# Performance work log

Measured on AMD Instinct MI355X. Metric: run time of the kernel, lower is better.

Reference implementation:

```python
import jax, jax.numpy as jnp
import numpy as np

N = 100000
E = 1600000
IN_DIM = 64
HID = 64


def _glorot(key, shape):
    fan_in, fan_out = shape[0], shape[1]
    lim = np.sqrt(6.0 / (fan_in + fan_out))
    return jax.random.uniform(key, shape, jnp.float32, -lim, lim)


def setup_inputs() -> dict:
    key = jax.random.key(0)
    ks = jax.random.split(key, 14)
    x = jax.random.normal(ks[0], (N, IN_DIM), jnp.float32)
    edge_index = jax.random.randint(ks[1], (2, E), 0, N, jnp.int64)
    dims = [(IN_DIM, HID), (HID, HID), (HID, HID), (HID, 1)]
    inp = {"x": x, "edge_index": edge_index}
    for i, (di, do) in enumerate(dims, start=1):
        inp[f"Wself{i}"] = _glorot(ks[2 + 3 * (i - 1)], (di, do))
        inp[f"Wneigh{i}"] = _glorot(ks[3 + 3 * (i - 1)], (di, do))
        inp[f"b{i}"] = jnp.zeros((do,), jnp.float32)
    return inp


def _gn_block(h, src, dst, deg_inv, Wself, Wneigh, b, act):
    # gather -> scatter-add -> mean -> dense transform (GraphConv-style)
    msg = h[src]                                           # [E, d]
    agg = jax.ops.segment_sum(msg, dst, num_segments=N)    # [N, d]
    agg = agg * deg_inv                                    # mean aggregation
    out = h @ Wself + agg @ Wneigh + b
    return act(out)


def reference(x, edge_index, Wself1, Wneigh1, b1, Wself2, Wneigh2, b2,
              Wself3, Wneigh3, b3, Wself4, Wneigh4, b4):
    src, dst = edge_index[0], edge_index[1]
    deg = jax.ops.segment_sum(jnp.ones((E,), x.dtype), dst, num_segments=N)
    deg_inv = (1.0 / jnp.maximum(deg, 1.0))[:, None]       # [N, 1]
    relu = jax.nn.relu
    h = _gn_block(x, src, dst, deg_inv, Wself1, Wneigh1, b1, relu)
    h = _gn_block(h, src, dst, deg_inv, Wself2, Wneigh2, b2, relu)
    h = _gn_block(h, src, dst, deg_inv, Wself3, Wneigh3, b3, relu)
    h = _gn_block(h, src, dst, deg_inv, Wself4, Wneigh4, b4, lambda z: z)
    return jax.nn.sigmoid(h)                               # [N, 1]
```

## Files before the change

kernel.cpp:

```cpp
#include <hip/hip_runtime.h>
#include <hip/hip_bf16.h>
#include <math.h>


using bfrag = __attribute__((ext_vector_type(8))) short;
using ffrag = __attribute__((ext_vector_type(4))) float;

#define BKT_SHIFT 9
#define BKT_NODES (1 << BKT_SHIFT)
#define AGG_F_STRIDE 65

__device__ __forceinline__ int load_idx32(const int* __restrict__ ei32, int is64,
                                          long long pos) {
    return is64 ? ei32[2 * pos] : ei32[pos];
}

__device__ __forceinline__ unsigned short f2b_rne(float f) {
    union { float f; unsigned u; } c;
    c.f = f;
    unsigned r = c.u + 0x7FFFu + ((c.u >> 16) & 1u);
    return (unsigned short)(r >> 16);
}

__device__ __forceinline__ float b2f(unsigned short u) {
    union { unsigned u; float f; } c;
    c.u = ((unsigned)u) << 16;
    return c.f;
}

__global__ void bprep_init_kernel(
    const float* __restrict__ Ws1, const float* __restrict__ Wn1,
    const float* __restrict__ Ws2, const float* __restrict__ Wn2,
    const float* __restrict__ Ws3, const float* __restrict__ Wn3,
    unsigned short* __restrict__ bthi, unsigned short* __restrict__ btlo,
    const int* __restrict__ ei, int* __restrict__ bktc, int* __restrict__ flag) {
    if (blockIdx.x == 0) {
        bktc[threadIdx.x] = 0;
        if (threadIdx.x == 0) {
            int allz = 1;
            for (int i = 0; i < 32; ++i)
                if (ei[2 * i + 1] != 0) allz = 0;
            *flag = allz;
        }
    }
    int i = blockIdx.x * 256 + threadIdx.x;
    if (i >= 3 * 8192) return;
    int layer = i >> 13;
    int j = i & 8191;
    int n = j >> 7, k = j & 127;
    const float* Ws = layer == 0 ? Ws1 : (layer == 1 ? Ws2 : Ws3);
    const float* Wn = layer == 0 ? Wn1 : (layer == 1 ? Wn2 : Wn3);
    float v = (k < 64) ? Ws[k * 64 + n] : Wn[(k - 64) * 64 + n];
    unsigned short hi = f2b_rne(v);
    bthi[i] = hi;
    btlo[i] = f2b_rne(v - b2f(hi));
}

__global__ void split_x_kernel(const float4* __restrict__ in, ushort4* __restrict__ hi,
                               int n4) {
    int i = blockIdx.x * blockDim.x + threadIdx.x;
    if (i >= n4) return;
    float4 v = in[i];
    ushort4 h;
    h.x = f2b_rne(v.x); h.y = f2b_rne(v.y); h.z = f2b_rne(v.z); h.w = f2b_rne(v.w);
    hi[i] = h;
}

__global__ __launch_bounds__(256) void binA_kernel(
    const int* __restrict__ ei32, const int* __restrict__ flagp,
    int* __restrict__ bktCnt, unsigned* __restrict__ bins, int E, int nbkt,
    int cap, int chunksz) {
    __shared__ int cnt[256];
    __shared__ int base[256];
    int is64 = *flagp;
    int elo = blockIdx.x * chunksz;
    int ehi = min(E, elo + chunksz);
    if (elo >= E) return;
    for (int i = threadIdx.x; i < nbkt; i += 256) cnt[i] = 0;
    __syncthreads();
    for (int e = elo + (int)threadIdx.x; e < ehi; e += 256) {
        int dst = load_idx32(ei32, is64, (long long)E + e);
        atomicAdd(&cnt[dst >> BKT_SHIFT], 1);
    }
    __syncthreads();
    for (int i = threadIdx.x; i < nbkt; i += 256) {
        base[i] = atomicAdd(&bktCnt[i], cnt[i]);
        cnt[i] = 0;
    }
    __syncthreads();
    for (int e = elo + (int)threadIdx.x; e < ehi; e += 256) {
        int dst = load_idx32(ei32, is64, (long long)E + e);
        int src = load_idx32(ei32, is64, e);
        int b = dst >> BKT_SHIFT;
        int r = atomicAdd(&cnt[b], 1);
        bins[(size_t)b * cap + base[b] + r] =
            ((unsigned)(dst & (BKT_NODES - 1)) << 23) | (unsigned)src;
    }
}

__global__ __launch_bounds__(256) void bucketCSR_kernel(
    const int* __restrict__ bktCnt, const unsigned* __restrict__ bins,
    int2* __restrict__ offp, int* __restrict__ col,
    float* __restrict__ dinv, int N, int cap) {
    __shared__ int deg[BKT_NODES];
    __shared__ int loc[BKT_NODES];
    __shared__ int ssum[256];
    int b = blockIdx.x;
    int lo = b << BKT_SHIFT;
    int n = min(BKT_NODES, N - lo);
    for (int i = threadIdx.x; i < BKT_NODES; i += 256) deg[i] = 0;
    __syncthreads();
    int cnt = bktCnt[b];
    const unsigned* bb = bins + (size_t)b * cap;
    for (int i = threadIdx.x; i < cnt; i += 256)
        atomicAdd(&deg[bb[i] >> 23], 1);
    __syncthreads();
    int t = threadIdx.x;
    int d0 = deg[2 * t], d1 = deg[2 * t + 1];
    int s = d0 + d1;
    ssum[t] = s;
    __syncthreads();
    for (int o = 1; o < 256; o <<= 1) {
        int v = (t >= o) ? ssum[t - o] : 0;
        __syncthreads();
        ssum[t] += v;
        __syncthreads();
    }
    int excl = ssum[t] - s;
    loc[2 * t] = excl;
    loc[2 * t + 1] = excl + d0;
    __syncthreads();
    int base = b * cap;
    for (int i = threadIdx.x; i < n; i += 256) {
        int d = deg[i];
        offp[lo + i] = make_int2(base + loc[i], base + loc[i] + d);
        dinv[lo + i] = 1.0f / fmaxf((float)d, 1.0f);
    }
    __syncthreads();
    for (int i = threadIdx.x; i < cnt; i += 256) {
        unsigned p = bb[i];
        int pos = atomicAdd(&loc[p >> 23], 1);
        col[base + pos] = (int)(p & 0x7FFFFFu);
    }
}

__device__ __forceinline__ void acc4(float4& a, ushort4 u) {
    a.x += b2f(u.x); a.y += b2f(u.y); a.z += b2f(u.z); a.w += b2f(u.w);
}

__device__ __forceinline__ void fma4(float4& a, float m, ushort4 u) {
    a.x = fmaf(m, b2f(u.x), a.x);
    a.y = fmaf(m, b2f(u.y), a.y);
    a.z = fmaf(m, b2f(u.z), a.z);
    a.w = fmaf(m, b2f(u.w), a.w);
}

__device__ __forceinline__ void gather_half(
    const unsigned short* __restrict__ Hhi, const int* __restrict__ col,
    float* __restrict__ dstF, int e, int end, int t16) {
    float4 a0 = make_float4(0.f, 0.f, 0.f, 0.f);
    float4 a1 = a0, a2 = a0, a3 = a0;
    const unsigned short* __restrict__ Hq = Hhi + t16 * 4;
    for (; e + 8 <= end; e += 8) {
        int s0 = col[e + 0], s1 = col[e + 1], s2 = col[e + 2], s3 = col[e + 3];
        int s4 = col[e + 4], s5 = col[e + 5], s6 = col[e + 6], s7 = col[e + 7];
        ushort4 u0 = *(const ushort4*)&Hq[(size_t)s0 * 64];
        ushort4 u1 = *(const ushort4*)&Hq[(size_t)s1 * 64];
        ushort4 u2 = *(const ushort4*)&Hq[(size_t)s2 * 64];
        ushort4 u3 = *(const ushort4*)&Hq[(size_t)s3 * 64];
        ushort4 u4 = *(const ushort4*)&Hq[(size_t)s4 * 64];
        ushort4 u5 = *(const ushort4*)&Hq[(size_t)s5 * 64];
        ushort4 u6 = *(const ushort4*)&Hq[(size_t)s6 * 64];
        ushort4 u7 = *(const ushort4*)&Hq[(size_t)s7 * 64];
        acc4(a0, u0); acc4(a1, u1); acc4(a2, u2); acc4(a3, u3);
        acc4(a0, u4); acc4(a1, u5); acc4(a2, u6); acc4(a3, u7);
    }
    int rem = end - e;
    if (rem > 0) {
        int last = end - 1;
#pragma unroll
        for (int j = 0; j < 7; ++j) {
            int idx = e + j;
            int cl = idx < last ? idx : last;
            int s = col[cl];
            ushort4 u = *(const ushort4*)&Hq[(size_t)s * 64];
            float m = (j < rem) ? 1.0f : 0.0f;
            if ((j & 3) == 0) fma4(a0, m, u);
            else if ((j & 3) == 1) fma4(a1, m, u);
            else if ((j & 3) == 2) fma4(a2, m, u);
            else fma4(a3, m, u);
        }
    }
    float4 s;
    s.x = (a0.x + a1.x) + (a2.x + a3.x);
    s.y = (a0.y + a1.y) + (a2.y + a3.y);
    s.z = (a0.z + a1.z) + (a2.z + a3.z);
    s.w = (a0.w + a1.w) + (a2.w + a3.w);
    *(float4*)&dstF[t16 * 4] = s;
}

__device__ __forceinline__ bfrag cvt8(const float* __restrict__ p0,
                                      const float* __restrict__ p1, float di) {
    bfrag r;
#pragma unroll
    for (int i = 0; i < 8; ++i)
        r[i] = (short)f2b_rne((p0[i] + p1[i]) * di);
    return r;
}

__global__ __launch_bounds__(512, 8) void layer_fused_kernel(
    const unsigned short* __restrict__ Hhi, const int2* __restrict__ offp,
    const int* __restrict__ col, const float* __restrict__ dinv,
    const unsigned short* __restrict__ Bthi, const unsigned short* __restrict__ Btlo,
    const float* __restrict__ b, unsigned short* __restrict__ Dhi, int N) {
    __shared__ float aggF[32 * AGG_F_STRIDE];
    int wave = threadIdx.x >> 6;
    int lane = threadIdx.x & 63;
    int g = lane >> 4;
    int t16 = lane & 15;
    int n0 = blockIdx.x * 16;
    int grp = wave * 4 + g;
    int li = grp >> 1, half = grp & 1;
    int n = n0 + li;
    int e0 = 0, e1 = 0;
    if (n < N) {
        int2 oo = offp[n];
        int d = oo.y - oo.x;
        int c0 = (d + 1) >> 1;
        e0 = half ? oo.x + c0 : oo.x;
        e1 = half ? oo.y : oo.x + c0;
    }
    gather_half(Hhi, col, &aggF[grp * AGG_F_STRIDE], e0, e1, t16);
    __syncthreads();
    if (wave < 4) {
        int m = t16, quad = g;
        int nr = n0 + m;
        if (nr > N - 1) nr = N - 1;
        float di = dinv[nr];
        const float* r0 = &aggF[(m * 2 + 0) * AGG_F_STRIDE];
        const float* r1 = &aggF[(m * 2 + 1) * AGG_F_STRIDE];
        const unsigned short* hrow = Hhi + (size_t)nr * 64 + quad * 8;
        bfrag ah[4];
        ah[0] = *(const bfrag*)(hrow);
        ah[1] = *(const bfrag*)(hrow + 32);
        ah[2] = cvt8(r0 + quad * 8, r1 + quad * 8, di);
        ah[3] = cvt8(r0 + 32 + quad * 8, r1 + 32 + quad * 8, di);
        int oc = wave * 16 + m;
        float bl = b[oc];
        ffrag acc = {bl, bl, bl, bl};
#pragma unroll
        for (int c = 0; c < 4; ++c) {
            bfrag bh = *(const bfrag*)(Bthi + (size_t)oc * 128 + c * 32 + quad * 8);
            bfrag bw = *(const bfrag*)(Btlo + (size_t)oc * 128 + c * 32 + quad * 8);
            acc = __builtin_amdgcn_mfma_f32_16x16x32_bf16(ah[c], bh, acc, 0, 0, 0);
            acc = __builtin_amdgcn_mfma_f32_16x16x32_bf16(ah[c], bw, acc, 0, 0, 0);
        }
#pragma unroll
        for (int r = 0; r < 4; ++r) {
            int node = n0 + quad * 4 + r;
            if (node < N)
                Dhi[(size_t)node * 64 + oc] = f2b_rne(fmaxf(acc[r], 0.f));
        }
    }
}

__global__ __launch_bounds__(512, 8) void layer_fused_last_kernel(
    const unsigned short* __restrict__ Hhi, const int2* __restrict__ offp,
    const int* __restrict__ col, const float* __restrict__ dinv,
    const unsigned short* __restrict__ Bthi, const unsigned short* __restrict__ Btlo,
    const float* __restrict__ b, const float* __restrict__ Ws4,
    const float* __restrict__ Wn4, float* __restrict__ sbuf,
    float* __restrict__ gbuf, int N) {
    __shared__ float aggF[32 * AGG_F_STRIDE];
    __shared__ float sPart[4][16];
    __shared__ float gPart[4][16];
    int wave = threadIdx.x >> 6;
    int lane = threadIdx.x & 63;
    int g = lane >> 4;
    int t16 = lane & 15;
    int n0 = blockIdx.x * 16;
    int grp = wave * 4 + g;
    int li = grp >> 1, half = grp & 1;
    int n = n0 + li;
    int e0 = 0, e1 = 0;
    if (n < N) {
        int2 oo = offp[n];
        int d = oo.y - oo.x;
        int c0 = (d + 1) >> 1;
        e0 = half ? oo.x + c0 : oo.x;
        e1 = half ? oo.y : oo.x + c0;
    }
    gather_half(Hhi, col, &aggF[grp * AGG_F_STRIDE], e0, e1, t16);
    __syncthreads();
    if (wave < 4) {
        int m = t16, quad = g;
        int nr = n0 + m;
        if (nr > N - 1) nr = N - 1;
        float di = dinv[nr];
        const float* r0 = &aggF[(m * 2 + 0) * AGG_F_STRIDE];
        const float* r1 = &aggF[(m * 2 + 1) * AGG_F_STRIDE];
        const unsigned short* hrow = Hhi + (size_t)nr * 64 + quad * 8;
        bfrag ah[4];
        ah[0] = *(const bfrag*)(hrow);
        ah[1] = *(const bfrag*)(hrow + 32);
        ah[2] = cvt8(r0 + quad * 8, r1 + quad * 8, di);
        ah[3] = cvt8(r0 + 32 + quad * 8, r1 + 32 + quad * 8, di);
        int oc = wave * 16 + m;
        float bl = b[oc];
        ffrag acc = {bl, bl, bl, bl};
#pragma unroll
        for (int c = 0; c < 4; ++c) {
            bfrag bh = *(const bfrag*)(Bthi + (size_t)oc * 128 + c * 32 + quad * 8);
            bfrag bw = *(const bfrag*)(Btlo + (size_t)oc * 128 + c * 32 + quad * 8);
            acc = __builtin_amdgcn_mfma_f32_16x16x32_bf16(ah[c], bh, acc, 0, 0, 0);
            acc = __builtin_amdgcn_mfma_f32_16x16x32_bf16(ah[c], bw, acc, 0, 0, 0);
        }
        float w4s = Ws4[oc], w4n = Wn4[oc];
#pragma unroll
        for (int r = 0; r < 4; ++r) {
            float v = fmaxf(acc[r], 0.f);
            float ps = v * w4s;
            float pg = v * w4n;
#pragma unroll
            for (int mask = 1; mask <= 8; mask <<= 1) {
                ps += __shfl_xor(ps, mask, 64);
                pg += __shfl_xor(pg, mask, 64);
            }
            if (m == 0) {
                sPart[wave][quad * 4 + r] = ps;
                gPart[wave][quad * 4 + r] = pg;
            }
        }
    }
    __syncthreads();
    if (threadIdx.x < 16) {
        int node = n0 + threadIdx.x;
        if (node < N) {
            float s = sPart[0][threadIdx.x] + sPart[1][threadIdx.x] +
                      sPart[2][threadIdx.x] + sPart[3][threadIdx.x];
            float gg = gPart[0][threadIdx.x] + gPart[1][threadIdx.x] +
                       gPart[2][threadIdx.x] + gPart[3][threadIdx.x];
            sbuf[node] = s;
            gbuf[node] = gg;
        }
    }
}

__global__ void final_kernel(const float* __restrict__ s, const float* __restrict__ dinv,
                             const float* __restrict__ g, const int2* __restrict__ offp,
                             const int* __restrict__ col,
                             const float* __restrict__ b4, float* __restrict__ out, int N) {
    int n = blockIdx.x * blockDim.x + threadIdx.x;
    if (n >= N) return;
    float a = 0.f;
    int2 oo = offp[n];
    for (int e = oo.x; e < oo.y; ++e) a += g[col[e]];
    float z = s[n] + dinv[n] * a + b4[0];
    out[n] = 1.0f / (1.0f + expf(-z));
}

static inline int cdiv(long long a, long long b) { return (int)((a + b - 1) / b); }

extern "C" void kernel_launch(void* const* d_in, const int* in_sizes, int n_in,
                              void* d_out, int out_size, void* d_ws, size_t ws_size,
                              hipStream_t stream) {
    const float* x   = (const float*)d_in[0];
    const int*   ei  = (const int*)d_in[1];
    const float* Ws1 = (const float*)d_in[2];
    const float* Wn1 = (const float*)d_in[3];
    const float* b1  = (const float*)d_in[4];
    const float* Ws2 = (const float*)d_in[5];
    const float* Wn2 = (const float*)d_in[6];
    const float* b2  = (const float*)d_in[7];
    const float* Ws3 = (const float*)d_in[8];
    const float* Wn3 = (const float*)d_in[9];
    const float* b3  = (const float*)d_in[10];
    const float* Ws4 = (const float*)d_in[11];
    const float* Wn4 = (const float*)d_in[12];
    const float* b4  = (const float*)d_in[13];
    float* out = (float*)d_out;

    const int N = in_sizes[0] / 64;
    const int E = in_sizes[1] / 2;

    const int nbkt = cdiv(N, BKT_NODES);
    int cap = E / nbkt + E / nbkt / 8 + 64;
    cap = (cap + 1) & ~1;

    unsigned* bins = (unsigned*)d_ws;
    int* col = (int*)(bins + (size_t)nbkt * cap);
    int2* offp = (int2*)(col + (size_t)nbkt * cap);
    unsigned short* HhiA = (unsigned short*)(offp + N);
    unsigned short* HhiB = HhiA + (size_t)N * 64;
    unsigned short* Bth  = HhiB + (size_t)N * 64;
    unsigned short* Btl  = Bth + 3 * 8192;
    float* dinv = (float*)(Btl + 3 * 8192);
    float* sbuf = dinv + N;
    float* gbuf = sbuf + N;
    int*   bktc = (int*)(gbuf + N);
    int*   flag = bktc + 256;

    const int BT = 256;
    const int gridN  = cdiv(N, BT);
    const int gridL  = cdiv(N, 16);
    const int binBlocks = 512;
    const int chunksz = cdiv(E, binBlocks);

    bprep_init_kernel<<<96, BT, 0, stream>>>(Ws1, Wn1, Ws2, Wn2, Ws3, Wn3,
                                             Bth, Btl, ei, bktc, flag);
    split_x_kernel<<<cdiv((long long)N * 16, BT), BT, 0, stream>>>(
        (const float4*)x, (ushort4*)HhiA, N * 16);

    binA_kernel<<<binBlocks, BT, 0, stream>>>(ei, flag, bktc, bins, E, nbkt, cap, chunksz);
    bucketCSR_kernel<<<nbkt, BT, 0, stream>>>(bktc, bins, offp, col, dinv, N, cap);

    layer_fused_kernel<<<gridL, 512, 0, stream>>>(HhiA, offp, col, dinv,
                                                  Bth, Btl, b1, HhiB, N);
    layer_fused_kernel<<<gridL, 512, 0, stream>>>(HhiB, offp, col, dinv,
                                                  Bth + 8192, Btl + 8192, b2, HhiA, N);
    layer_fused_last_kernel<<<gridL, 512, 0, stream>>>(HhiA, offp, col, dinv,
                                                       Bth + 16384, Btl + 16384, b3,
                                                       Ws4, Wn4, sbuf, gbuf, N);

    final_kernel<<<gridN, BT, 0, stream>>>(sbuf, dinv, gbuf, offp, col, b4, out, N);
}
```

Baseline: 343.2 us.

## Replace bucketed binning CSR build with global histogram, scan, atomic scatter

Swaps the two-pass bucket-binning CSR construction (shared-memory bucket counts, staged bins array, per-bucket local sort) for a plain global-degree histogram, a two-level prefix scan, and an atomic-cursor scatter into col. This drops the intermediate bins buffer and its extra read/write pass. In exchange it adds more kernel launches and relies on global atomics spread across many destinations, which can contend. The order of neighbours within each row becomes nondeterministic, and the scattered writes no longer stay within a bucket's region, so the layer kernels may see less favourable locality.

```diff
diff --git a/kernel.cpp b/kernel.cpp
--- a/kernel.cpp
+++ b/kernel.cpp
@@ -6,8 +6,6 @@
 using bfrag = __attribute__((ext_vector_type(8))) short;
 using ffrag = __attribute__((ext_vector_type(4))) float;
 
-#define BKT_SHIFT 9
-#define BKT_NODES (1 << BKT_SHIFT)
 #define AGG_F_STRIDE 65
 
 __device__ __forceinline__ int load_idx32(const int* __restrict__ ei32, int is64,
@@ -28,20 +26,20 @@
     return c.f;
 }
 
-__global__ void bprep_init_kernel(
+__global__ __launch_bounds__(256) void bprep_init_kernel(
     const float* __restrict__ Ws1, const float* __restrict__ Wn1,
     const float* __restrict__ Ws2, const float* __restrict__ Wn2,
     const float* __restrict__ Ws3, const float* __restrict__ Wn3,
     unsigned short* __restrict__ bthi, unsigned short* __restrict__ btlo,
-    const int* __restrict__ ei, int* __restrict__ bktc, int* __restrict__ flag) {
-    if (blockIdx.x == 0) {
-        bktc[threadIdx.x] = 0;
-        if (threadIdx.x == 0) {
-            int allz = 1;
-            for (int i = 0; i < 32; ++i)
-                if (ei[2 * i + 1] != 0) allz = 0;
-            *flag = allz;
-        }
+    const int* __restrict__ ei, int* __restrict__ deg, int* __restrict__ flag,
+    int N) {
+    for (int j = blockIdx.x * 256 + threadIdx.x; j < N; j += gridDim.x * 256)
+        deg[j] = 0;
+    if (blockIdx.x == 0 && threadIdx.x == 0) {
+        int allz = 1;
+        for (int i = 0; i < 32; ++i)
+            if (ei[2 * i + 1] != 0) allz = 0;
+        *flag = allz;
     }
     int i = blockIdx.x * 256 + threadIdx.x;
     if (i >= 3 * 8192) return;
@@ -56,8 +54,8 @@
     btlo[i] = f2b_rne(v - b2f(hi));
 }
 
-__global__ void split_x_kernel(const float4* __restrict__ in, ushort4* __restrict__ hi,
-                               int n4) {
+__global__ __launch_bounds__(256) void split_x_kernel(
+    const float4* __restrict__ in, ushort4* __restrict__ hi, int n4) {
     int i = blockIdx.x * blockDim.x + threadIdx.x;
     if (i >= n4) return;
     float4 v = in[i];
@@ -66,81 +64,73 @@
     hi[i] = h;
 }
 
-__global__ __launch_bounds__(256) void binA_kernel(
+__global__ __launch_bounds__(256) void hist_kernel(
     const int* __restrict__ ei32, const int* __restrict__ flagp,
-    int* __restrict__ bktCnt, unsigned* __restrict__ bins, int E, int nbkt,
-    int cap, int chunksz) {
-    __shared__ int cnt[256];
-    __shared__ int base[256];
+    int* __restrict__ deg, int E) {
     int is64 = *flagp;
-    int elo = blockIdx.x * chunksz;
-    int ehi = min(E, elo + chunksz);
-    if (elo >= E) return;
-    for (int i = threadIdx.x; i < nbkt; i += 256) cnt[i] = 0;
+    for (int e = blockIdx.x * 256 + threadIdx.x; e < E; e += gridDim.x * 256) {
+        int dst = load_idx32(ei32, is64, (long long)E + e);
+        atomicAdd(&deg[dst], 1);
+    }
+}
+
+__global__ __launch_bounds__(512) void scan1_kernel(
+    const int* __restrict__ deg, int* __restrict__ locOff,
+    int* __restrict__ btot, int N) {
+    __shared__ int s[512];
+    int b = blockIdx.x, t = threadIdx.x;
+    int n = b * 512 + t;
+    int d = (n < N) ? deg[n] : 0;
+    s[t] = d;
     __syncthreads();
-    for (int e = elo + (int)threadIdx.x; e < ehi; e += 256) {
-        int dst = load_idx32(ei32, is64, (long long)E + e);
-        atomicAdd(&cnt[dst >> BKT_SHIFT], 1);
-    }
-    __syncthreads();
-    for (int i = threadIdx.x; i < nbkt; i += 256) {
-        base[i] = atomicAdd(&bktCnt[i], cnt[i]);
-        cnt[i] = 0;
-    }
-    __syncthreads();
-    for (int e = elo + (int)threadIdx.x; e < ehi; e += 256) {
-        int dst = load_idx32(ei32, is64, (long long)E + e);
-        int src = load_idx32(ei32, is64, e);
-        int b = dst >> BKT_SHIFT;
-        int r = atomicAdd(&cnt[b], 1);
-        bins[(size_t)b * cap + base[b] + r] =
-            ((unsigned)(dst & (BKT_NODES - 1)) << 23) | (unsigned)src;
-    }
-}
-
-__global__ __launch_bounds__(256) void bucketCSR_kernel(
-    const int* __restrict__ bktCnt, const unsigned* __restrict__ bins,
-    int2* __restrict__ offp, int* __restrict__ col,
-    float* __restrict__ dinv, int N, int cap) {
-    __shared__ int deg[BKT_NODES];
-    __shared__ int loc[BKT_NODES];
-    __shared__ int ssum[256];
-    int b = blockIdx.x;
-    int lo = b << BKT_SHIFT;
-    int n = min(BKT_NODES, N - lo);
-    for (int i = threadIdx.x; i < BKT_NODES; i += 256) deg[i] = 0;
-    __syncthreads();
-    int cnt = bktCnt[b];
-    const unsigned* bb = bins + (size_t)b * cap;
-    for (int i = threadIdx.x; i < cnt; i += 256)
-        atomicAdd(&deg[bb[i] >> 23], 1);
-    __syncthreads();
+    for (int o = 1; o < 512; o <<= 1) {
+        int v = (t >= o) ? s[t - o] : 0;
+        __syncthreads();
+        s[t] += v;
+        __syncthreads();
+    }
+    if (n < N) locOff[n] = s[t] - d;
+    if (t == 511) btot[b] = s[t];
+}
+
+__global__ __launch_bounds__(256) void scan2_kernel(
+    const int* __restrict__ btot, int* __restrict__ bbase, int nb) {
+    __shared__ int s[256];
     int t = threadIdx.x;
-    int d0 = deg[2 * t], d1 = deg[2 * t + 1];
-    int s = d0 + d1;
-    ssum[t] = s;
+    int d = (t < nb) ? btot[t] : 0;
+    s[t] = d;
     __syncthreads();
     for (int o = 1; o < 256; o <<= 1) {
-        int v = (t >= o) ? ssum[t - o] : 0;
+        int v = (t >= o) ? s[t - o] : 0;
         __syncthreads();
-        ssum[t] += v;
+        s[t] += v;
         __syncthreads();
     }
-    int excl = ssum[t] - s;
-    loc[2 * t] = excl;
-    loc[2 * t + 1] = excl + d0;
-    __syncthreads();
-    int base = b * cap;
-    for (int i = threadIdx.x; i < n; i += 256) {
-        int d = deg[i];
-        offp[lo + i] = make_int2(base + loc[i], base + loc[i] + d);
-        dinv[lo + i] = 1.0f / fmaxf((float)d, 1.0f);
-    }
-    __syncthreads();
-    for (int i = threadIdx.x; i < cnt; i += 256) {
-        unsigned p = bb[i];
-        int pos = atomicAdd(&loc[p >> 23], 1);
-        col[base + pos] = (int)(p & 0x7FFFFFu);
+    if (t < nb) bbase[t] = s[t] - d;
+}
+
+__global__ __launch_bounds__(256) void finalize_kernel(
+    const int* __restrict__ deg, const int* __restrict__ locOff,
+    const int* __restrict__ bbase, int2* __restrict__ offp,
+    int* __restrict__ cur, float* __restrict__ dinv, int N) {
+    int n = blockIdx.x * 256 + threadIdx.x;
+    if (n >= N) return;
+    int d = deg[n];
+    int start = locOff[n] + bbase[n >> 9];
+    offp[n] = make_int2(start, start + d);
+    cur[n] = start;
+    dinv[n] = 1.0f / fmaxf((float)d, 1.0f);
+}
+
+__global__ __launch_bounds__(256) void scatter_kernel(
+    const int* __restrict__ ei32, const int* __restrict__ flagp,
+    int* __restrict__ cur, int* __restrict__ col, int E) {
+    int is64 = *flagp;
+    for (int e = blockIdx.x * 256 + threadIdx.x; e < E; e += gridDim.x * 256) {
+        int src = load_idx32(ei32, is64, e);
+        int dst = load_idx32(ei32, is64, (long long)E + e);
+        int p = atomicAdd(&cur[dst], 1);
+        col[p] = src;
     }
 }
 
@@ -346,10 +336,11 @@
     }
 }
 
-__global__ void final_kernel(const float* __restrict__ s, const float* __restrict__ dinv,
-                             const float* __restrict__ g, const int2* __restrict__ offp,
-                             const int* __restrict__ col,
-                             const float* __restrict__ b4, float* __restrict__ out, int N) {
+__global__ __launch_bounds__(256) void final_kernel(
+    const float* __restrict__ s, const float* __restrict__ dinv,
+    const float* __restrict__ g, const int2* __restrict__ offp,
+    const int* __restrict__ col,
+    const float* __restrict__ b4, float* __restrict__ out, int N) {
     int n = blockIdx.x * blockDim.x + threadIdx.x;
     if (n >= N) return;
     float a = 0.f;
@@ -382,37 +373,39 @@
 
     const int N = in_sizes[0] / 64;
     const int E = in_sizes[1] / 2;
-
-    const int nbkt = cdiv(N, BKT_NODES);
-    int cap = E / nbkt + E / nbkt / 8 + 64;
-    cap = (cap + 1) & ~1;
-
-    unsigned* bins = (unsigned*)d_ws;
-    int* col = (int*)(bins + (size_t)nbkt * cap);
-    int2* offp = (int2*)(col + (size_t)nbkt * cap);
-    unsigned short* HhiA = (unsigned short*)(offp + N);
+    const int nb512 = cdiv(N, 512);
+
+    int2* offp = (int2*)d_ws;
+    int* col   = (int*)(offp + N);
+    unsigned short* HhiA = (unsigned short*)(col + E);
     unsigned short* HhiB = HhiA + (size_t)N * 64;
     unsigned short* Bth  = HhiB + (size_t)N * 64;
     unsigned short* Btl  = Bth + 3 * 8192;
     float* dinv = (float*)(Btl + 3 * 8192);
     float* sbuf = dinv + N;
     float* gbuf = sbuf + N;
-    int*   bktc = (int*)(gbuf + N);
-    int*   flag = bktc + 256;
+    int*   deg    = (int*)(gbuf + N);
+    int*   locOff = deg + N;
+    int*   cur    = locOff + N;
+    int*   btot   = cur + N;
+    int*   bbase  = btot + 256;
+    int*   flag   = bbase + 256;
 
     const int BT = 256;
     const int gridN  = cdiv(N, BT);
     const int gridL  = cdiv(N, 16);
-    const int binBlocks = 512;
-    const int chunksz = cdiv(E, binBlocks);
-
-    bprep_init_kernel<<<96, BT, 0, stream>>>(Ws1, Wn1, Ws2, Wn2, Ws3, Wn3,
-                                             Bth, Btl, ei, bktc, flag);
+    const int gridE  = min(2048, cdiv(E, BT));
+
+    bprep_init_kernel<<<128, BT, 0, stream>>>(Ws1, Wn1, Ws2, Wn2, Ws3, Wn3,
+                                              Bth, Btl, ei, deg, flag, N);
     split_x_kernel<<<cdiv((long long)N * 16, BT), BT, 0, stream>>>(
         (const float4*)x, (ushort4*)HhiA, N * 16);
 
-    binA_kernel<<<binBlocks, BT, 0, stream>>>(ei, flag, bktc, bins, E, nbkt, cap, chunksz);
-    bucketCSR_kernel<<<nbkt, BT, 0, stream>>>(bktc, bins, offp, col, dinv, N, cap);
+    hist_kernel<<<gridE, BT, 0, stream>>>(ei, flag, deg, E);
+    scan1_kernel<<<nb512, 512, 0, stream>>>(deg, locOff, btot, N);
+    scan2_kernel<<<1, BT, 0, stream>>>(btot, bbase, nb512);
+    finalize_kernel<<<gridN, BT, 0, stream>>>(deg, locOff, bbase, offp, cur, dinv, N);
+    scatter_kernel<<<gridE, BT, 0, stream>>>(ei, flag, cur, col, E);
 
     layer_fused_kernel<<<gridL, 512, 0, stream>>>(HhiA, offp, col, dinv,
                                                   Bth, Btl, b1, HhiB, N);
```

Measured after the change: 510.3 us. +48.7%, slower.
